# Optimization experiments

Hardware: AMD Instinct MI355X
Metric: run time of the kernel (lower is better)

Reference implementation:

```python
import jax, jax.numpy as jnp
import numpy as np

BN_EPS = 1e-3


def _knn_group(p1, p2, k):
    # p1, p2: [N, 3]. For each point in p1 find k nearest in p2.
    d2 = (jnp.sum(p1 * p1, -1)[:, None] + jnp.sum(p2 * p2, -1)[None, :]
          - 2.0 * (p1 @ p2.T))                      # [N, N]
    _, idx = jax.lax.top_k(-d2, k)                   # [N, k]
    nn = p2[idx]                                     # [N, k, 3]
    resi = nn - p1[:, None, :]                       # [N, k, 3]
    dist = jnp.linalg.norm(resi, axis=-1, keepdims=True)
    feat = jnp.concatenate([resi, dist], axis=-1)    # [N, k, 4]
    return feat, nn


def _conv_bn_relu(x, W, b, g, be):
    # x: [B, Cin, N, K]; 1x1 conv == channel matmul, BN uses batch stats (train mode)
    y = jnp.einsum('oi,binK->bonK', W, x) + b[None, :, None, None]
    m = jnp.mean(y, axis=(0, 2, 3), keepdims=True)
    v = jnp.var(y, axis=(0, 2, 3), keepdims=True)
    y = g[None, :, None, None] * (y - m) * jax.lax.rsqrt(v + BN_EPS) + be[None, :, None, None]
    return jax.nn.relu(y)


def setup_inputs() -> dict:
    key = jax.random.key(0)
    ks = jax.random.split(key, 8)
    B, N, k = 4, 4096, 32
    C = [4, 64, 64, 128]
    inp = {
        'points1': jax.random.normal(ks[0], (B, 3, N), jnp.float32),
        'points2': jax.random.normal(ks[1], (B, 3, N), jnp.float32),
        'k': k,
        't': jax.random.uniform(ks[2], (B,), jnp.float32),
    }
    for i in range(3):
        kw = jax.random.fold_in(ks[3], i)
        inp[f'W{i+1}'] = jax.random.normal(kw, (C[i + 1], C[i]), jnp.float32) * (1.0 / np.sqrt(C[i]))
        inp[f'b{i+1}'] = jnp.zeros((C[i + 1],), jnp.float32)
        inp[f'g{i+1}'] = jnp.ones((C[i + 1],), jnp.float32)
        inp[f'be{i+1}'] = jnp.zeros((C[i + 1],), jnp.float32)
    return inp


def reference(points1, points2, k, t, W1, b1, g1, be1, W2, b2, g2, be2, W3, b3, g3, be3):
    p1 = jnp.transpose(points1, (0, 2, 1))           # [B, N, 3]
    p2 = jnp.transpose(points2, (0, 2, 1))
    knn = jax.vmap(_knn_group, in_axes=(0, 0, None))
    f1, nn1 = knn(p1, p1, k)                          # [B, N, k, 4], [B, N, k, 3]
    f2, nn2 = knn(p1, p2, k)
    feats = jnp.concatenate([f1, f2], axis=2)         # [B, N, 2k, 4]
    grouped = jnp.concatenate([nn1, nn2], axis=2)     # [B, N, 2k, 3]
    x = jnp.transpose(feats, (0, 3, 1, 2))            # [B, 4, N, 2k]
    x = _conv_bn_relu(x, W1, b1, g1, be1)
    x = _conv_bn_relu(x, W2, b2, g2, be2)
    x = _conv_bn_relu(x, W3, b3, g3, be3)             # [B, 128, N, 2k]
    scores = jnp.max(x, axis=1)                       # [B, N, 2k]
    w = jax.nn.softmax(scores, axis=-1)               # [B, N, 2k]
    fused = jnp.einsum('bnk,bnkc->bcn', w, grouped)   # [B, 3, N]
    return fused
```

## Files before the change

### kernel.cpp

```cpp
#include <hip/hip_runtime.h>
#include <hip/hip_bf16.h>

#define B_   4
#define N_   4096
#define KNN_ 32
#define KK_  64
#define MTOT 1048576
#define BN_EPS 1e-3f

typedef unsigned int u32;
typedef unsigned long long u64;
typedef __attribute__((ext_vector_type(8))) short bf16x8;
typedef __attribute__((ext_vector_type(4))) float f32x4;

__device__ __forceinline__ ushort f2bf_bits(float f) {
    u32 b = __float_as_uint(f);
    b += 0x7fffu + ((b >> 16) & 1u);
    return (ushort)(b >> 16);
}

__global__ __launch_bounds__(256, 3) void knn_kernel(
    const float* __restrict__ p1, const float* __restrict__ p2,
    float* __restrict__ feats)
{
    __shared__ float2 cxy[N_];
    __shared__ float  cz[N_];

    const int tid  = threadIdx.x;
    const int wave = tid >> 6, lane = tid & 63;
    const int pb    = blockIdx.x / 96;
    const int chunk = blockIdx.x % 96;
    const int pr = pb >> 2, b = pb & 3;
    const int start = (chunk * 4096) / 96;
    const int end   = ((chunk + 1) * 4096) / 96;

    const float* srcb = (pr ? p2 : p1) + (size_t)b * 3 * N_;
    for (int n = tid; n < N_; n += 256) {
        float x = srcb[n], y = srcb[N_ + n], z = srcb[2*N_ + n];
        cxy[n] = make_float2(x, y);
        cz[n]  = z;
    }
    __syncthreads();

    const float* p1b = p1 + (size_t)b * 3 * N_;
    const u64 below = (1ull << lane) - 1ull;

    for (int n = start + wave; n < end; n += 4) {
        float qx, qy, qz;
        if (pr == 0) { float2 q = cxy[n]; qx = q.x; qy = q.y; qz = cz[n]; }
        else         { qx = p1b[n]; qy = p1b[N_ + n]; qz = p1b[2*N_ + n]; }
        const float s1 = fmaf(qx, qx, fmaf(qy, qy, qz*qz));

        u32 keys[64];
        u32 a0 = 0xFFFFFFFFu, a1 = 0xFFFFFFFFu, a2 = 0xFFFFFFFFu, a3 = 0xFFFFFFFFu;
        u32 b0 = 0xFFFFFFFFu, b1 = 0xFFFFFFFFu, b2 = 0xFFFFFFFFu, b3 = 0xFFFFFFFFu;
        #pragma unroll
        for (int j = 0; j < 32; ++j) {
            {
                float2 cA = cxy[j * 64 + lane];
                float  zA = cz[j * 64 + lane];
                float cw  = fmaf(cA.x, cA.x, fmaf(cA.y, cA.y, zA*zA));
                float dot = fmaf(qx, cA.x, fmaf(qy, cA.y, qz * zA));
                float d2  = fmaf(-2.0f, dot, s1 + cw);
                u32 u = __float_as_uint(d2);
                u32 key = u ^ (u32)(((int)u >> 31) | 0x80000000);
                keys[j] = key;
                a3 = min(a3, key);
                u32 t;
                t = min(a2, a3); a3 = max(a2, a3); a2 = t;
                t = min(a1, a2); a2 = max(a1, a2); a1 = t;
                t = min(a0, a1); a1 = max(a0, a1); a0 = t;
            }
            {
                float2 cB = cxy[(j + 32) * 64 + lane];
                float  zB = cz[(j + 32) * 64 + lane];
                float cw  = fmaf(cB.x, cB.x, fmaf(cB.y, cB.y, zB*zB));
                float dot = fmaf(qx, cB.x, fmaf(qy, cB.y, qz * zB));
                float d2  = fmaf(-2.0f, dot, s1 + cw);
                u32 u = __float_as_uint(d2);
                u32 key = u ^ (u32)(((int)u >> 31) | 0x80000000);
                keys[j + 32] = key;
                b3 = min(b3, key);
                u32 t;
                t = min(b2, b3); b3 = max(b2, b3); b2 = t;
                t = min(b1, b2); b2 = max(b1, b2); b1 = t;
                t = min(b0, b1); b1 = max(b0, b1); b0 = t;
            }
        }
        u32 k0 = a0, k1 = a1, k2 = a2, k3 = a3;
        #pragma unroll
        for (int m = 0; m < 4; ++m) {
            u32 x = (m == 0) ? b0 : (m == 1) ? b1 : (m == 2) ? b2 : b3;
            k3 = min(k3, x);
            u32 t;
            t = min(k2, k3); k3 = max(k2, k3); k2 = t;
            t = min(k1, k2); k2 = max(k1, k2); k1 = t;
            t = min(k0, k1); k1 = max(k0, k1); k0 = t;
        }

        u32 mn = k0, mx = k3;
        #pragma unroll
        for (int off = 1; off < 64; off <<= 1) {
            mn = min(mn, (u32)__shfl_xor((int)mn, off, 64));
            mx = max(mx, (u32)__shfl_xor((int)mx, off, 64));
        }
        u32 lo = mn, hi = mx;
        while (lo < hi) {
            u32 mid = lo + ((hi - lo) >> 1);
            int c = __popcll(__ballot(k0 <= mid)) + __popcll(__ballot(k1 <= mid))
                  + __popcll(__ballot(k2 <= mid)) + __popcll(__ballot(k3 <= mid));
            if (c >= 32) hi = mid; else lo = mid + 1;
        }
        u32 T = lo;

        int nl;
        if (__ballot(k3 <= T) == 0ull) {
            nl = __popcll(__ballot(k0 < T)) + __popcll(__ballot(k1 < T))
               + __popcll(__ballot(k2 < T)) + __popcll(__ballot(k3 < T));
        } else {
            nl = 0;
            #pragma unroll
            for (int j = 0; j < 64; ++j) nl += __popcll(__ballot(keys[j] < T));
            if (nl > 31) {
                lo = 0u; hi = T;
                while (lo < hi) {
                    u32 mid = lo + ((hi - lo) >> 1);
                    int c = 0;
                    #pragma unroll
                    for (int j = 0; j < 64; ++j) c += __popcll(__ballot(keys[j] <= mid));
                    if (c >= 32) hi = mid; else lo = mid + 1;
                }
                T = lo;
                nl = 0;
                #pragma unroll
                for (int j = 0; j < 64; ++j) nl += __popcll(__ballot(keys[j] < T));
            }
        }
        const int need_eq = 32 - nl;

        float* fout = feats + ((size_t)(b * N_ + n) * KK_ + pr * KNN_) * 4;
        int base = 0, eq_seen = 0;
        #pragma unroll
        for (int j = 0; j < 64; ++j) {
            u32 key = keys[j];
            bool lt = key < T;
            bool eq = key == T;
            u64 mlt = __ballot(lt);
            u64 meq = __ballot(eq);
            if (mlt | meq) {
                int slot = -1;
                if (lt) slot = base + __popcll(mlt & below);
                else if (eq) {
                    int es = eq_seen + __popcll(meq & below);
                    if (es < need_eq) slot = nl + es;
                }
                if (slot >= 0) {
                    float2 cx2 = cxy[j * 64 + lane];
                    float  cz1 = cz[j * 64 + lane];
                    float rx = cx2.x - qx, ry = cx2.y - qy, rz = cz1 - qz;
                    float dist = sqrtf(fmaf(rx, rx, fmaf(ry, ry, rz*rz)));
                    *(float4*)(fout + slot * 4) = make_float4(rx, ry, rz, dist);
                }
                base    += __popcll(mlt);
                eq_seen += __popcll(meq);
            }
        }
    }
}

__global__ __launch_bounds__(256) void moments_kernel(
    const float4* __restrict__ feats4, float* __restrict__ mom)
{
    __shared__ float part[4][14];
    const int tid = threadIdx.x, lane = tid & 63, wv = tid >> 6;
    float a[14];
    #pragma unroll
    for (int s = 0; s < 14; ++s) a[s] = 0.f;
    for (int idx = blockIdx.x * 256 + tid; idx < MTOT; idx += 256 * 256) {
        float4 f = feats4[idx];
        a[0] += f.x; a[1] += f.y; a[2] += f.z; a[3] += f.w;
        a[4]  = fmaf(f.x, f.x, a[4]);  a[5]  = fmaf(f.x, f.y, a[5]);
        a[6]  = fmaf(f.x, f.z, a[6]);  a[7]  = fmaf(f.x, f.w, a[7]);
        a[8]  = fmaf(f.y, f.y, a[8]);  a[9]  = fmaf(f.y, f.z, a[9]);
        a[10] = fmaf(f.y, f.w, a[10]); a[11] = fmaf(f.z, f.z, a[11]);
        a[12] = fmaf(f.z, f.w, a[12]); a[13] = fmaf(f.w, f.w, a[13]);
    }
    #pragma unroll
    for (int s = 0; s < 14; ++s) {
        #pragma unroll
        for (int off = 1; off < 64; off <<= 1) a[s] += __shfl_xor(a[s], off, 64);
    }
    if (lane == 0) {
        #pragma unroll
        for (int s = 0; s < 14; ++s) part[wv][s] = a[s];
    }
    __syncthreads();
    if (tid < 14) {
        float v = part[0][tid] + part[1][tid] + part[2][tid] + part[3][tid];
        atomicAdd(&mom[tid * 16], v);
    }
}

__global__ __launch_bounds__(256) void conv2_mfma(
    const float* __restrict__ feats,
    const float* __restrict__ W1,
    const float* __restrict__ g1, const float* __restrict__ be1,
    const float* __restrict__ W2,
    const float* __restrict__ mom,
    ushort* __restrict__ y2F, float* __restrict__ s2S, float* __restrict__ s2Q)
{
    __shared__ float statS[64], statQ[64];
    const int tid = threadIdx.x;
    const int wid = tid >> 6, l = tid & 63, q = l >> 4, i = l & 15;
    if (tid < 64) { statS[tid] = 0.f; statQ[tid] = 0.f; }

    const float invM = 1.0f / MTOT;
    const float M0 = mom[0*16], M1 = mom[1*16], M2 = mom[2*16], M3 = mom[3*16];
    const float Sxx = mom[4*16],  Sxy = mom[5*16],  Sxz = mom[6*16],  Sxd = mom[7*16];
    const float Syy = mom[8*16],  Syz = mom[9*16],  Syd = mom[10*16];
    const float Szz = mom[11*16], Szd = mom[12*16], Sdd = mom[13*16];

    float4 w1f[16];
    float  c1v[16];
    #pragma unroll
    for (int h = 0; h < 2; ++h)
      #pragma unroll
      for (int j = 0; j < 8; ++j) {
        int ci = h*32 + q*8 + j;
        float w0 = W1[ci*4+0], w1 = W1[ci*4+1], w2 = W1[ci*4+2], w3 = W1[ci*4+3];
        float meanf = (w0*M0 + w1*M1 + w2*M2 + w3*M3) * invM;
        float qq = w0*(w0*Sxx + 2.f*(w1*Sxy + w2*Sxz + w3*Sxd))
                 + w1*(w1*Syy + 2.f*(w2*Syz + w3*Syd))
                 + w2*(w2*Szz + 2.f*w3*Szd)
                 + w3*w3*Sdd;
        float var = qq * invM - meanf * meanf;
        float sc  = g1[ci] * rsqrtf(var + BN_EPS);
        w1f[h*8+j] = make_float4(sc*w0, sc*w1, sc*w2, sc*w3);
        c1v[h*8+j] = fmaf(-sc, meanf, be1[ci]);
      }
    bf16x8 a2[4][2];
    #pragma unroll
    for (int t = 0; t < 4; ++t)
      #pragma unroll
      for (int h = 0; h < 2; ++h)
        #pragma unroll
        for (int j = 0; j < 8; ++j)
          a2[t][h][j] = (short)f2bf_bits(W2[(t*16 + i)*64 + h*32 + q*8 + j]);

    float ssum[16], ssq[16];
    #pragma unroll
    for (int s = 0; s < 16; ++s) { ssum[s] = 0.f; ssq[s] = 0.f; }
    __syncthreads();

    for (int r16 = 0; r16 < 16; ++r16) {
        const int row = blockIdx.x * 16 + r16;
        float4 f = ((const float4*)feats)[row*64 + wid*16 + i];
        bf16x8 xb[2];
        #pragma unroll
        for (int h = 0; h < 2; ++h)
          #pragma unroll
          for (int j = 0; j < 8; ++j) {
            float4 w = w1f[h*8+j];
            float x = fmaxf(fmaf(w.x, f.x, fmaf(w.y, f.y, fmaf(w.z, f.z, fmaf(w.w, f.w, c1v[h*8+j])))), 0.f);
            xb[h][j] = (short)f2bf_bits(x);
          }
        f32x4 acc[4];
        #pragma unroll
        for (int t = 0; t < 4; ++t) acc[t] = (f32x4){0.f,0.f,0.f,0.f};
        #pragma unroll
        for (int t = 0; t < 4; ++t) {
            acc[t] = __builtin_amdgcn_mfma_f32_16x16x32_bf16(a2[t][0], xb[0], acc[t], 0, 0, 0);
            acc[t] = __builtin_amdgcn_mfma_f32_16x16x32_bf16(a2[t][1], xb[1], acc[t], 0, 0, 0);
        }
        ushort* wp = y2F + row*4096 + wid*1024 + q*64 + i*4;
        #pragma unroll
        for (int t = 0; t < 4; ++t) {
            #pragma unroll
            for (int reg = 0; reg < 4; ++reg) {
                float y = acc[t][reg];
                ssum[t*4+reg] += y;
                ssq[t*4+reg]  = fmaf(y, y, ssq[t*4+reg]);
            }
            uint2 pk;
            pk.x = (u32)f2bf_bits(acc[t][0]) | ((u32)f2bf_bits(acc[t][1]) << 16);
            pk.y = (u32)f2bf_bits(acc[t][2]) | ((u32)f2bf_bits(acc[t][3]) << 16);
            *(uint2*)(wp + t*256) = pk;
        }
    }
    #pragma unroll
    for (int s = 0; s < 16; ++s) {
        #pragma unroll
        for (int off = 1; off < 16; off <<= 1) {
            ssum[s] += __shfl_xor(ssum[s], off, 64);
            ssq[s]  += __shfl_xor(ssq[s],  off, 64);
        }
    }
    if (i == 0) {
        #pragma unroll
        for (int s = 0; s < 16; ++s) {
            int co = (s >> 2)*16 + q*4 + (s & 3);
            atomicAdd(&statS[co], ssum[s]);
            atomicAdd(&statQ[co], ssq[s]);
        }
    }
    __syncthreads();
    if (tid < 64) { atomicAdd(&s2S[tid], statS[tid]); atomicAdd(&s2Q[tid], statQ[tid]); }
}

template<bool FINAL>
__global__ __launch_bounds__(256) void conv3_mfma(
    const ushort* __restrict__ y2F,
    const float* __restrict__ g2, const float* __restrict__ be2,
    const float* __restrict__ W3,
    const float* __restrict__ g3, const float* __restrict__ be3,
    const float* __restrict__ s2S, const float* __restrict__ s2Q,
    float* __restrict__ s3S, float* __restrict__ s3Q,
    const float4* __restrict__ feats4, const float* __restrict__ p1,
    float* __restrict__ outp)
{
    __shared__ float statS[128], statQ[128];
    __shared__ float sc3L[128], sh3L[128];
    __shared__ float scoreL[2][64];

    const int tid = threadIdx.x;
    const int wid = tid >> 6, l = tid & 63, q = l >> 4, i = l & 15;

    if (!FINAL) {
        if (tid < 128) { statS[tid] = 0.f; statQ[tid] = 0.f; }
    } else if (tid < 128) {
        float m  = s3S[tid] * (1.0f / MTOT);
        float v  = s3Q[tid] * (1.0f / MTOT) - m * m;
        float sc = g3[tid] * rsqrtf(v + BN_EPS);
        sc3L[tid] = sc;
        sh3L[tid] = fmaf(-sc, m, be3[tid]);
    }

    float sc2v[16], sh2v[16];
    #pragma unroll
    for (int h = 0; h < 2; ++h)
      #pragma unroll
      for (int j = 0; j < 8; ++j) {
        int ci = h*32 + q*8 + j;
        float m  = s2S[ci] * (1.0f / MTOT);
        float v  = s2Q[ci] * (1.0f / MTOT) - m * m;
        float sc = g2[ci] * rsqrtf(v + BN_EPS);
        sc2v[h*8+j] = sc;
        sh2v[h*8+j] = fmaf(-sc, m, be2[ci]);
      }
    bf16x8 a3[8][2];
    #pragma unroll
    for (int t = 0; t < 8; ++t)
      #pragma unroll
      for (int h = 0; h < 2; ++h)
        #pragma unroll
        for (int j = 0; j < 8; ++j)
          a3[t][h][j] = (short)f2bf_bits(W3[(t*16 + i)*64 + h*32 + q*8 + j]);

    float ssum[32], ssq[32];
    if (!FINAL) {
        #pragma unroll
        for (int s = 0; s < 32; ++s) { ssum[s] = 0.f; ssq[s] = 0.f; }
    }
    __syncthreads();

    for (int r16 = 0; r16 < 16; ++r16) {
        const int row = blockIdx.x * 16 + r16;
        const ushort* rp = y2F + row*4096 + wid*1024 + q*128 + i*4;
        uint2 u00 = *(const uint2*)(rp);
        uint2 u01 = *(const uint2*)(rp + 64);
        uint2 u10 = *(const uint2*)(rp + 512);
        uint2 u11 = *(const uint2*)(rp + 576);

        bf16x8 xb[2];
        #pragma unroll
        for (int h = 0; h < 2; ++h) {
            u32 w0 = (h == 0) ? u00.x : u10.x;
            u32 w1 = (h == 0) ? u00.y : u10.y;
            u32 w2 = (h == 0) ? u01.x : u11.x;
            u32 w3 = (h == 0) ? u01.y : u11.y;
            float xf[8];
            xf[0] = __uint_as_float(w0 << 16); xf[1] = __uint_as_float(w0 & 0xffff0000u);
            xf[2] = __uint_as_float(w1 << 16); xf[3] = __uint_as_float(w1 & 0xffff0000u);
            xf[4] = __uint_as_float(w2 << 16); xf[5] = __uint_as_float(w2 & 0xffff0000u);
            xf[6] = __uint_as_float(w3 << 16); xf[7] = __uint_as_float(w3 & 0xffff0000u);
            #pragma unroll
            for (int j = 0; j < 8; ++j) {
                float x = fmaxf(fmaf(sc2v[h*8+j], xf[j], sh2v[h*8+j]), 0.f);
                xb[h][j] = (short)f2bf_bits(x);
            }
        }
        f32x4 acc[8];
        #pragma unroll
        for (int t = 0; t < 8; ++t) acc[t] = (f32x4){0.f,0.f,0.f,0.f};
        #pragma unroll
        for (int t = 0; t < 8; ++t) {
            acc[t] = __builtin_amdgcn_mfma_f32_16x16x32_bf16(a3[t][0], xb[0], acc[t], 0, 0, 0);
            acc[t] = __builtin_amdgcn_mfma_f32_16x16x32_bf16(a3[t][1], xb[1], acc[t], 0, 0, 0);
        }

        if (!FINAL) {
            #pragma unroll
            for (int t = 0; t < 8; ++t)
              #pragma unroll
              for (int reg = 0; reg < 4; ++reg) {
                float y = acc[t][reg];
                ssum[t*4+reg] += y;
                ssq[t*4+reg]  = fmaf(y, y, ssq[t*4+reg]);
              }
        } else {
            float mx = -3.4e38f;
            #pragma unroll
            for (int t = 0; t < 8; ++t) {
                float4 s4 = *(const float4*)&sc3L[t*16 + q*4];
                float4 h4 = *(const float4*)&sh3L[t*16 + q*4];
                mx = fmaxf(mx, fmaf(s4.x, acc[t][0], h4.x));
                mx = fmaxf(mx, fmaf(s4.y, acc[t][1], h4.y));
                mx = fmaxf(mx, fmaf(s4.z, acc[t][2], h4.z));
                mx = fmaxf(mx, fmaf(s4.w, acc[t][3], h4.w));
            }
            mx = fmaxf(mx, __shfl_xor(mx, 16, 64));
            mx = fmaxf(mx, __shfl_xor(mx, 32, 64));
            mx = fmaxf(mx, 0.f);
            if (q == 0) scoreL[r16 & 1][wid*16 + i] = mx;
            __syncthreads();
            if (wid == 0) {
                float sc = scoreL[r16 & 1][l];
                float m2 = sc;
                #pragma unroll
                for (int off = 1; off < 64; off <<= 1) m2 = fmaxf(m2, __shfl_xor(m2, off, 64));
                float e = __expf(sc - m2);
                float se = e;
                #pragma unroll
                for (int off = 1; off < 64; off <<= 1) se += __shfl_xor(se, off, 64);
                float w = e / se;
                const int bb = row >> 12, n = row & 4095;
                float qx = p1[(size_t)bb*3*N_ + n];
                float qy = p1[(size_t)bb*3*N_ + N_ + n];
                float qz = p1[(size_t)bb*3*N_ + 2*N_ + n];
                float4 f4 = feats4[row*64 + l];
                float ox = w * (f4.x + qx), oy = w * (f4.y + qy), oz = w * (f4.z + qz);
                #pragma unroll
                for (int off = 1; off < 64; off <<= 1) {
                    ox += __shfl_xor(ox, off, 64);
                    oy += __shfl_xor(oy, off, 64);
                    oz += __shfl_xor(oz, off, 64);
                }
                if (l == 0) {
                    outp[bb*3*N_ + 0*N_ + n] = ox;
                    outp[bb*3*N_ + 1*N_ + n] = oy;
                    outp[bb*3*N_ + 2*N_ + n] = oz;
                }
            }
        }
    }

    if (!FINAL) {
        #pragma unroll
        for (int s = 0; s < 32; ++s) {
            #pragma unroll
            for (int off = 1; off < 16; off <<= 1) {
                ssum[s] += __shfl_xor(ssum[s], off, 64);
                ssq[s]  += __shfl_xor(ssq[s],  off, 64);
            }
        }
        if (i == 0) {
            #pragma unroll
            for (int s = 0; s < 32; ++s) {
                int co = (s >> 2)*16 + q*4 + (s & 3);
                atomicAdd(&statS[co], ssum[s]);
                atomicAdd(&statQ[co], ssq[s]);
            }
        }
        __syncthreads();
        if (tid < 128) { atomicAdd(&s3S[tid], statS[tid]); atomicAdd(&s3Q[tid], statQ[tid]); }
    }
}

extern "C" void kernel_launch(void* const* d_in, const int* in_sizes, int n_in,
                              void* d_out, int out_size, void* d_ws, size_t ws_size,
                              hipStream_t stream)
{
    const float* p1  = (const float*)d_in[0];
    const float* p2  = (const float*)d_in[1];
    const float* W1  = (const float*)d_in[4];
    const float* g1  = (const float*)d_in[6];
    const float* be1 = (const float*)d_in[7];
    const float* W2  = (const float*)d_in[8];
    const float* g2  = (const float*)d_in[10];
    const float* be2 = (const float*)d_in[11];
    const float* W3  = (const float*)d_in[12];
    const float* g3  = (const float*)d_in[14];
    const float* be3 = (const float*)d_in[15];

    char* ws = (char*)d_ws;
    const size_t OFF_FEATS = 4096;
    const size_t OFF_Y2    = OFF_FEATS + (size_t)MTOT * 4 * 4;
    const size_t NEEDED    = OFF_Y2 + (size_t)MTOT * 64 * 2;
    if (ws_size < NEEDED) return;

    float* s2S = (float*)(ws + 512);  float* s2Q = (float*)(ws + 768);
    float* s3S = (float*)(ws + 1024); float* s3Q = (float*)(ws + 1536);
    float* mom = (float*)(ws + 2048);
    float* feats   = (float*)(ws + OFF_FEATS);
    ushort* y2F    = (ushort*)(ws + OFF_Y2);

    hipMemsetAsync(ws, 0, 4096, stream);

    knn_kernel<<<768, 256, 0, stream>>>(p1, p2, feats);
    moments_kernel<<<256, 256, 0, stream>>>((const float4*)feats, mom);
    conv2_mfma<<<1024, 256, 0, stream>>>(feats, W1, g1, be1, W2, mom,
                                         y2F, s2S, s2Q);
    conv3_mfma<false><<<1024, 256, 0, stream>>>(y2F, g2, be2, W3, g3, be3,
                                                s2S, s2Q, s3S, s3Q,
                                                nullptr, nullptr, nullptr);
    conv3_mfma<true><<<1024, 256, 0, stream>>>(y2F, g2, be2, W3, g3, be3,
                                               s2S, s2Q, s3S, s3Q,
                                               (const float4*)feats, p1,
                                               (float*)d_out);
}
```

Measured before the change: 512.8 us.

## Recompute conv2 output from feats instead of materializing bf16 y2 buffer

Drops the 128MB bf16 intermediate for layer-2 activations. The first pass now only accumulates BN2 statistics, and both layer-3 passes recompute conv1 and conv2 from the compact 4-channel feats. The per-channel BN1-folded weights move into shared memory, and W3 columns are permuted to match the MFMA output layout so the conv2 result feeds conv3 directly from registers. This trades global memory traffic for repeated MFMA and ALU work on conv2.

```diff
diff --git a/kernel.cpp b/kernel.cpp
--- a/kernel.cpp
+++ b/kernel.cpp
@@ -201,43 +201,57 @@
     }
 }
 
-__global__ __launch_bounds__(256) void conv2_mfma(
-    const float* __restrict__ feats,
-    const float* __restrict__ W1,
-    const float* __restrict__ g1, const float* __restrict__ be1,
-    const float* __restrict__ W2,
+__device__ __forceinline__ void build_w1L(
+    int tid, const float* __restrict__ W1, const float* __restrict__ g1,
+    const float* __restrict__ be1, const float* __restrict__ mom,
+    float4* w1L, float* c1L)
+{
+    if (tid < 64) {
+        const float invM = 1.0f / MTOT;
+        int ci = tid;
+        float w0 = W1[ci*4+0], w1 = W1[ci*4+1], w2 = W1[ci*4+2], w3 = W1[ci*4+3];
+        float meanf = (w0*mom[0] + w1*mom[16] + w2*mom[32] + w3*mom[48]) * invM;
+        float qq = w0*(w0*mom[64] + 2.f*(w1*mom[80] + w2*mom[96] + w3*mom[112]))
+                 + w1*(w1*mom[128] + 2.f*(w2*mom[144] + w3*mom[160]))
+                 + w2*(w2*mom[176] + 2.f*w3*mom[192])
+                 + w3*w3*mom[208];
+        float var = qq * invM - meanf * meanf;
+        float sc  = g1[ci] * rsqrtf(var + BN_EPS);
+        w1L[ci] = make_float4(sc*w0, sc*w1, sc*w2, sc*w3);
+        c1L[ci] = fmaf(-sc, meanf, be1[ci]);
+    }
+}
+
+__device__ __forceinline__ void build_xb2(
+    float4 f, int q, const float4* w1L, const float* c1L, bf16x8 xb2[2])
+{
+    #pragma unroll
+    for (int h = 0; h < 2; ++h)
+      #pragma unroll
+      for (int j = 0; j < 8; ++j) {
+        int ci = h*32 + q*8 + j;
+        float4 w = w1L[ci];
+        float x = fmaxf(fmaf(w.x, f.x, fmaf(w.y, f.y, fmaf(w.z, f.z,
+                       fmaf(w.w, f.w, c1L[ci])))), 0.f);
+        xb2[h][j] = (short)f2bf_bits(x);
+      }
+}
+
+__global__ __launch_bounds__(256) void p1_kernel(
+    const float4* __restrict__ feats4,
+    const float* __restrict__ W1, const float* __restrict__ g1,
+    const float* __restrict__ be1, const float* __restrict__ W2,
     const float* __restrict__ mom,
-    ushort* __restrict__ y2F, float* __restrict__ s2S, float* __restrict__ s2Q)
-{
+    float* __restrict__ s2S, float* __restrict__ s2Q)
+{
+    __shared__ float4 w1L[64];
+    __shared__ float  c1L[64];
     __shared__ float statS[64], statQ[64];
     const int tid = threadIdx.x;
     const int wid = tid >> 6, l = tid & 63, q = l >> 4, i = l & 15;
     if (tid < 64) { statS[tid] = 0.f; statQ[tid] = 0.f; }
-
-    const float invM = 1.0f / MTOT;
-    const float M0 = mom[0*16], M1 = mom[1*16], M2 = mom[2*16], M3 = mom[3*16];
-    const float Sxx = mom[4*16],  Sxy = mom[5*16],  Sxz = mom[6*16],  Sxd = mom[7*16];
-    const float Syy = mom[8*16],  Syz = mom[9*16],  Syd = mom[10*16];
-    const float Szz = mom[11*16], Szd = mom[12*16], Sdd = mom[13*16];
-
-    float4 w1f[16];
-    float  c1v[16];
-    #pragma unroll
-    for (int h = 0; h < 2; ++h)
-      #pragma unroll
-      for (int j = 0; j < 8; ++j) {
-        int ci = h*32 + q*8 + j;
-        float w0 = W1[ci*4+0], w1 = W1[ci*4+1], w2 = W1[ci*4+2], w3 = W1[ci*4+3];
-        float meanf = (w0*M0 + w1*M1 + w2*M2 + w3*M3) * invM;
-        float qq = w0*(w0*Sxx + 2.f*(w1*Sxy + w2*Sxz + w3*Sxd))
-                 + w1*(w1*Syy + 2.f*(w2*Syz + w3*Syd))
-                 + w2*(w2*Szz + 2.f*w3*Szd)
-                 + w3*w3*Sdd;
-        float var = qq * invM - meanf * meanf;
-        float sc  = g1[ci] * rsqrtf(var + BN_EPS);
-        w1f[h*8+j] = make_float4(sc*w0, sc*w1, sc*w2, sc*w3);
-        c1v[h*8+j] = fmaf(-sc, meanf, be1[ci]);
-      }
+    build_w1L(tid, W1, g1, be1, mom, w1L, c1L);
+
     bf16x8 a2[4][2];
     #pragma unroll
     for (int t = 0; t < 4; ++t)
@@ -254,37 +268,20 @@
 
     for (int r16 = 0; r16 < 16; ++r16) {
         const int row = blockIdx.x * 16 + r16;
-        float4 f = ((const float4*)feats)[row*64 + wid*16 + i];
-        bf16x8 xb[2];
-        #pragma unroll
-        for (int h = 0; h < 2; ++h)
-          #pragma unroll
-          for (int j = 0; j < 8; ++j) {
-            float4 w = w1f[h*8+j];
-            float x = fmaxf(fmaf(w.x, f.x, fmaf(w.y, f.y, fmaf(w.z, f.z, fmaf(w.w, f.w, c1v[h*8+j])))), 0.f);
-            xb[h][j] = (short)f2bf_bits(x);
-          }
-        f32x4 acc[4];
-        #pragma unroll
-        for (int t = 0; t < 4; ++t) acc[t] = (f32x4){0.f,0.f,0.f,0.f};
+        float4 f = feats4[row*64 + wid*16 + i];
+        bf16x8 xb2[2];
+        build_xb2(f, q, w1L, c1L, xb2);
         #pragma unroll
         for (int t = 0; t < 4; ++t) {
-            acc[t] = __builtin_amdgcn_mfma_f32_16x16x32_bf16(a2[t][0], xb[0], acc[t], 0, 0, 0);
-            acc[t] = __builtin_amdgcn_mfma_f32_16x16x32_bf16(a2[t][1], xb[1], acc[t], 0, 0, 0);
-        }
-        ushort* wp = y2F + row*4096 + wid*1024 + q*64 + i*4;
-        #pragma unroll
-        for (int t = 0; t < 4; ++t) {
+            f32x4 a = (f32x4){0.f,0.f,0.f,0.f};
+            a = __builtin_amdgcn_mfma_f32_16x16x32_bf16(a2[t][0], xb2[0], a, 0, 0, 0);
+            a = __builtin_amdgcn_mfma_f32_16x16x32_bf16(a2[t][1], xb2[1], a, 0, 0, 0);
             #pragma unroll
             for (int reg = 0; reg < 4; ++reg) {
-                float y = acc[t][reg];
+                float y = a[reg];
                 ssum[t*4+reg] += y;
                 ssq[t*4+reg]  = fmaf(y, y, ssq[t*4+reg]);
             }
-            uint2 pk;
-            pk.x = (u32)f2bf_bits(acc[t][0]) | ((u32)f2bf_bits(acc[t][1]) << 16);
-            pk.y = (u32)f2bf_bits(acc[t][2]) | ((u32)f2bf_bits(acc[t][3]) << 16);
-            *(uint2*)(wp + t*256) = pk;
         }
     }
     #pragma unroll
@@ -308,53 +305,65 @@
 }
 
 template<bool FINAL>
-__global__ __launch_bounds__(256) void conv3_mfma(
-    const ushort* __restrict__ y2F,
+__global__ __launch_bounds__(256) void p23_kernel(
+    const float4* __restrict__ feats4,
+    const float* __restrict__ W1, const float* __restrict__ g1,
+    const float* __restrict__ be1, const float* __restrict__ W2,
+    const float* __restrict__ mom,
     const float* __restrict__ g2, const float* __restrict__ be2,
     const float* __restrict__ W3,
     const float* __restrict__ g3, const float* __restrict__ be3,
     const float* __restrict__ s2S, const float* __restrict__ s2Q,
     float* __restrict__ s3S, float* __restrict__ s3Q,
-    const float4* __restrict__ feats4, const float* __restrict__ p1,
-    float* __restrict__ outp)
-{
+    const float* __restrict__ p1, float* __restrict__ outp)
+{
+    __shared__ float4 w1L[64];
+    __shared__ float  c1L[64];
     __shared__ float statS[128], statQ[128];
-    __shared__ float sc3L[128], sh3L[128];
     __shared__ float scoreL[2][64];
 
     const int tid = threadIdx.x;
     const int wid = tid >> 6, l = tid & 63, q = l >> 4, i = l & 15;
 
+    build_w1L(tid, W1, g1, be1, mom, w1L, c1L);
     if (!FINAL) {
         if (tid < 128) { statS[tid] = 0.f; statQ[tid] = 0.f; }
     } else if (tid < 128) {
         float m  = s3S[tid] * (1.0f / MTOT);
         float v  = s3Q[tid] * (1.0f / MTOT) - m * m;
         float sc = g3[tid] * rsqrtf(v + BN_EPS);
-        sc3L[tid] = sc;
-        sh3L[tid] = fmaf(-sc, m, be3[tid]);
+        statS[tid] = sc;
+        statQ[tid] = fmaf(-sc, m, be3[tid]);
     }
 
     float sc2v[16], sh2v[16];
     #pragma unroll
-    for (int h = 0; h < 2; ++h)
+    for (int s = 0; s < 16; ++s) {
+        int ch = (s >> 2)*16 + q*4 + (s & 3);
+        float m  = s2S[ch] * (1.0f / MTOT);
+        float v  = s2Q[ch] * (1.0f / MTOT) - m * m;
+        float sc = g2[ch] * rsqrtf(v + BN_EPS);
+        sc2v[s] = sc;
+        sh2v[s] = fmaf(-sc, m, be2[ch]);
+    }
+    bf16x8 a2[4][2];
+    #pragma unroll
+    for (int t = 0; t < 4; ++t)
       #pragma unroll
-      for (int j = 0; j < 8; ++j) {
-        int ci = h*32 + q*8 + j;
-        float m  = s2S[ci] * (1.0f / MTOT);
-        float v  = s2Q[ci] * (1.0f / MTOT) - m * m;
-        float sc = g2[ci] * rsqrtf(v + BN_EPS);
-        sc2v[h*8+j] = sc;
-        sh2v[h*8+j] = fmaf(-sc, m, be2[ci]);
-      }
+      for (int h = 0; h < 2; ++h)
+        #pragma unroll
+        for (int j = 0; j < 8; ++j)
+          a2[t][h][j] = (short)f2bf_bits(W2[(t*16 + i)*64 + h*32 + q*8 + j]);
     bf16x8 a3[8][2];
     #pragma unroll
     for (int t = 0; t < 8; ++t)
       #pragma unroll
       for (int h = 0; h < 2; ++h)
         #pragma unroll
-        for (int j = 0; j < 8; ++j)
-          a3[t][h][j] = (short)f2bf_bits(W3[(t*16 + i)*64 + h*32 + q*8 + j]);
+        for (int j = 0; j < 8; ++j) {
+          int ch = (2*h + (j >> 2))*16 + q*4 + (j & 3);
+          a3[t][h][j] = (short)f2bf_bits(W3[(t*16 + i)*64 + ch]);
+        }
 
     float ssum[32], ssq[32];
     if (!FINAL) {
@@ -365,58 +374,53 @@
 
     for (int r16 = 0; r16 < 16; ++r16) {
         const int row = blockIdx.x * 16 + r16;
-        const ushort* rp = y2F + row*4096 + wid*1024 + q*128 + i*4;
-        uint2 u00 = *(const uint2*)(rp);
-        uint2 u01 = *(const uint2*)(rp + 64);
-        uint2 u10 = *(const uint2*)(rp + 512);
-        uint2 u11 = *(const uint2*)(rp + 576);
-
-        bf16x8 xb[2];
-        #pragma unroll
-        for (int h = 0; h < 2; ++h) {
-            u32 w0 = (h == 0) ? u00.x : u10.x;
-            u32 w1 = (h == 0) ? u00.y : u10.y;
-            u32 w2 = (h == 0) ? u01.x : u11.x;
-            u32 w3 = (h == 0) ? u01.y : u11.y;
-            float xf[8];
-            xf[0] = __uint_as_float(w0 << 16); xf[1] = __uint_as_float(w0 & 0xffff0000u);
-            xf[2] = __uint_as_float(w1 << 16); xf[3] = __uint_as_float(w1 & 0xffff0000u);
-            xf[4] = __uint_as_float(w2 << 16); xf[5] = __uint_as_float(w2 & 0xffff0000u);
-            xf[6] = __uint_as_float(w3 << 16); xf[7] = __uint_as_float(w3 & 0xffff0000u);
-            #pragma unroll
-            for (int j = 0; j < 8; ++j) {
-                float x = fmaxf(fmaf(sc2v[h*8+j], xf[j], sh2v[h*8+j]), 0.f);
-                xb[h][j] = (short)f2bf_bits(x);
-            }
-        }
-        f32x4 acc[8];
-        #pragma unroll
-        for (int t = 0; t < 8; ++t) acc[t] = (f32x4){0.f,0.f,0.f,0.f};
-        #pragma unroll
-        for (int t = 0; t < 8; ++t) {
-            acc[t] = __builtin_amdgcn_mfma_f32_16x16x32_bf16(a3[t][0], xb[0], acc[t], 0, 0, 0);
-            acc[t] = __builtin_amdgcn_mfma_f32_16x16x32_bf16(a3[t][1], xb[1], acc[t], 0, 0, 0);
-        }
+        float4 f = feats4[row*64 + wid*16 + i];
+        bf16x8 xb2[2];
+        build_xb2(f, q, w1L, c1L, xb2);
+        f32x4 acc2[4];
+        #pragma unroll
+        for (int t = 0; t < 4; ++t) {
+            f32x4 a = (f32x4){0.f,0.f,0.f,0.f};
+            a = __builtin_amdgcn_mfma_f32_16x16x32_bf16(a2[t][0], xb2[0], a, 0, 0, 0);
+            a = __builtin_amdgcn_mfma_f32_16x16x32_bf16(a2[t][1], xb2[1], a, 0, 0, 0);
+            acc2[t] = a;
+        }
+        bf16x8 xb3[2];
+        #pragma unroll
+        for (int h = 0; h < 2; ++h)
+          #pragma unroll
+          for (int j = 0; j < 8; ++j) {
+            int t = 2*h + (j >> 2), reg = j & 3, s = t*4 + reg;
+            float x = fmaxf(fmaf(sc2v[s], acc2[t][reg], sh2v[s]), 0.f);
+            xb3[h][j] = (short)f2bf_bits(x);
+          }
 
         if (!FINAL) {
             #pragma unroll
-            for (int t = 0; t < 8; ++t)
-              #pragma unroll
-              for (int reg = 0; reg < 4; ++reg) {
-                float y = acc[t][reg];
-                ssum[t*4+reg] += y;
-                ssq[t*4+reg]  = fmaf(y, y, ssq[t*4+reg]);
-              }
+            for (int t = 0; t < 8; ++t) {
+                f32x4 a = (f32x4){0.f,0.f,0.f,0.f};
+                a = __builtin_amdgcn_mfma_f32_16x16x32_bf16(a3[t][0], xb3[0], a, 0, 0, 0);
+                a = __builtin_amdgcn_mfma_f32_16x16x32_bf16(a3[t][1], xb3[1], a, 0, 0, 0);
+                #pragma unroll
+                for (int reg = 0; reg < 4; ++reg) {
+                    float y = a[reg];
+                    ssum[t*4+reg] += y;
+                    ssq[t*4+reg]  = fmaf(y, y, ssq[t*4+reg]);
+                }
+            }
         } else {
             float mx = -3.4e38f;
             #pragma unroll
             for (int t = 0; t < 8; ++t) {
-                float4 s4 = *(const float4*)&sc3L[t*16 + q*4];
-                float4 h4 = *(const float4*)&sh3L[t*16 + q*4];
-                mx = fmaxf(mx, fmaf(s4.x, acc[t][0], h4.x));
-                mx = fmaxf(mx, fmaf(s4.y, acc[t][1], h4.y));
-                mx = fmaxf(mx, fmaf(s4.z, acc[t][2], h4.z));
-                mx = fmaxf(mx, fmaf(s4.w, acc[t][3], h4.w));
+                f32x4 a = (f32x4){0.f,0.f,0.f,0.f};
+                a = __builtin_amdgcn_mfma_f32_16x16x32_bf16(a3[t][0], xb3[0], a, 0, 0, 0);
+                a = __builtin_amdgcn_mfma_f32_16x16x32_bf16(a3[t][1], xb3[1], a, 0, 0, 0);
+                float4 s4 = *(const float4*)&statS[t*16 + q*4];
+                float4 h4 = *(const float4*)&statQ[t*16 + q*4];
+                mx = fmaxf(mx, fmaf(s4.x, a[0], h4.x));
+                mx = fmaxf(mx, fmaf(s4.y, a[1], h4.y));
+                mx = fmaxf(mx, fmaf(s4.z, a[2], h4.z));
+                mx = fmaxf(mx, fmaf(s4.w, a[3], h4.w));
             }
             mx = fmaxf(mx, __shfl_xor(mx, 16, 64));
             mx = fmaxf(mx, __shfl_xor(mx, 32, 64));
@@ -494,27 +498,25 @@
 
     char* ws = (char*)d_ws;
     const size_t OFF_FEATS = 4096;
-    const size_t OFF_Y2    = OFF_FEATS + (size_t)MTOT * 4 * 4;
-    const size_t NEEDED    = OFF_Y2 + (size_t)MTOT * 64 * 2;
+    const size_t NEEDED    = OFF_FEATS + (size_t)MTOT * 4 * 4;
     if (ws_size < NEEDED) return;
 
     float* s2S = (float*)(ws + 512);  float* s2Q = (float*)(ws + 768);
     float* s3S = (float*)(ws + 1024); float* s3Q = (float*)(ws + 1536);
     float* mom = (float*)(ws + 2048);
-    float* feats   = (float*)(ws + OFF_FEATS);
-    ushort* y2F    = (ushort*)(ws + OFF_Y2);
+    float* feats = (float*)(ws + OFF_FEATS);
 
     hipMemsetAsync(ws, 0, 4096, stream);
 
     knn_kernel<<<768, 256, 0, stream>>>(p1, p2, feats);
     moments_kernel<<<256, 256, 0, stream>>>((const float4*)feats, mom);
-    conv2_mfma<<<1024, 256, 0, stream>>>(feats, W1, g1, be1, W2, mom,
-                                         y2F, s2S, s2Q);
-    conv3_mfma<false><<<1024, 256, 0, stream>>>(y2F, g2, be2, W3, g3, be3,
-                                                s2S, s2Q, s3S, s3Q,
-                                                nullptr, nullptr, nullptr);
-    conv3_mfma<true><<<1024, 256, 0, stream>>>(y2F, g2, be2, W3, g3, be3,
-                                               s2S, s2Q, s3S, s3Q,
-                                               (const float4*)feats, p1,
+    p1_kernel<<<1024, 256, 0, stream>>>((const float4*)feats, W1, g1, be1, W2,
+                                        mom, s2S, s2Q);
+    p23_kernel<false><<<1024, 256, 0, stream>>>((const float4*)feats, W1, g1, be1,
+                                                W2, mom, g2, be2, W3, g3, be3,
+                                                s2S, s2Q, s3S, s3Q, nullptr, nullptr);
+    p23_kernel<true><<<1024, 256, 0, stream>>>((const float4*)feats, W1, g1, be1,
+                                               W2, mom, g2, be2, W3, g3, be3,
+                                               s2S, s2Q, s3S, s3Q, p1,
                                                (float*)d_out);
 }
```

Measured after the change: 620.3 us. +21.0%, slower.
